# Kernel optimization log

Measured on AMD Instinct MI355X. Metric: run time of the kernel, lower is better.

The kernel has to match this reference:

```python
import jax, jax.numpy as jnp
import numpy as np

N = 100000  # number of nodes
E = 1600000  # number of edges (before self-loops)
D_IN, D_HID, D_OUT = 128, 128, 64


def gcn_conv(x, src, dst, W, b):
    """One PyG-style GCNConv: x' = D^{-1/2} A_hat D^{-1/2} (x W) + b, with self-loops in src/dst."""
    h = x @ W  # [N, D_out]
    deg = jax.ops.segment_sum(jnp.ones(src.shape[0], dtype=h.dtype), dst, num_segments=N)
    dinv = jnp.where(deg > 0, jax.lax.rsqrt(deg), 0.0)
    norm = dinv[src] * dinv[dst]  # [E+N]
    msgs = h[src] * norm[:, None]  # gather + scale
    out = jax.ops.segment_sum(msgs, dst, num_segments=N)  # scatter-add
    return out + b


def setup_inputs() -> dict:
    key = jax.random.key(0)
    k1, k2, k3, k4 = jax.random.split(key, 4)
    x = jax.random.normal(k1, (N, D_IN), dtype=jnp.float32)
    edge_index = jax.random.randint(k2, (2, E), 0, N, dtype=jnp.int64)
    W1 = jax.random.normal(k3, (D_IN, D_HID), dtype=jnp.float32) * (1.0 / np.sqrt(D_IN))
    b1 = jnp.zeros((D_HID,), dtype=jnp.float32)
    W2 = jax.random.normal(k4, (D_HID, D_OUT), dtype=jnp.float32) * (1.0 / np.sqrt(D_HID))
    b2 = jnp.zeros((D_OUT,), dtype=jnp.float32)
    return {"x": x, "edge_index": edge_index, "W1": W1, "b1": b1, "W2": W2, "b2": b2}


def reference(x, edge_index, W1, b1, W2, b2):
    # add self-loops once (GCNConv default add_self_loops=True)
    loops = jnp.arange(N, dtype=edge_index.dtype)
    src = jnp.concatenate([edge_index[0], loops])
    dst = jnp.concatenate([edge_index[1], loops])
    h = jax.nn.relu(gcn_conv(x, src, dst, W1, b1))
    out = gcn_conv(h, src, dst, W2, b2)
    return out
```

## Files before the change

kernel.cpp:

```cpp
#include <hip/hip_runtime.h>


#define NN 100000
#define EE 1600000
#define NB 391
#define BCAP 4608
#define PCAP 6656
#define EPB 8192
#define PBLK ((EE + EPB - 1) / EPB)

typedef _Float16 f16;
typedef _Float16 f16x8 __attribute__((ext_vector_type(8)));
typedef _Float16 f16x4 __attribute__((ext_vector_type(4)));
typedef float f32x4 __attribute__((ext_vector_type(4)));

__device__ __forceinline__ int load_idx(const void* p, long long i, int is64) {
    if (is64) return (int)((const long long*)p)[i];
    return ((const int*)p)[i];
}

__global__ void init_buckets(int* cursor) {
    int i = blockIdx.x * 256 + threadIdx.x;
    if (i < NB) cursor[i] = i * BCAP;
}

__global__ __launch_bounds__(256) void partition_kernel(const void* ei,
                                                        int* __restrict__ cursor,
                                                        unsigned* __restrict__ col32) {
    __shared__ int lh[NB], lbase[NB], lfill[NB];
    __shared__ int s_is64;
    for (int i = threadIdx.x; i < NB; i += 256) { lh[i] = 0; lfill[i] = 0; }
    if (threadIdx.x == 0) {
        const unsigned* w = (const unsigned*)ei;
        unsigned acc = 0;
        #pragma unroll
        for (int k = 0; k < 8; k++) acc |= w[2 * (k * 997 + 1) + 1];
        s_is64 = (acc == 0);
    }
    __syncthreads();
    int is64 = s_is64;
    long long base = (long long)blockIdx.x * EPB;
    #pragma unroll 4
    for (int k = 0; k < EPB / 256; k++) {
        long long i = base + k * 256 + threadIdx.x;
        if (i < EE) {
            int d = load_idx(ei, (long long)EE + i, is64);
            atomicAdd(&lh[d >> 8], 1);
        }
    }
    __syncthreads();
    for (int i = threadIdx.x; i < NB; i += 256)
        lbase[i] = lh[i] ? atomicAdd(&cursor[i], lh[i]) : 0;
    __syncthreads();
    #pragma unroll 4
    for (int k = 0; k < EPB / 256; k++) {
        long long i = base + k * 256 + threadIdx.x;
        if (i < EE) {
            int s = load_idx(ei, i, is64);
            int d = load_idx(ei, (long long)EE + i, is64);
            int b = d >> 8;
            int r = atomicAdd(&lfill[b], 1);
            col32[lbase[b] + r] = ((unsigned)s << 8) | (unsigned)(d & 255);
        }
    }
}

__global__ __launch_bounds__(256) void bucket_fill_kernel(const unsigned* __restrict__ col32,
                                                          const int* __restrict__ cursor,
                                                          int2* __restrict__ rsp,
                                                          float* __restrict__ dinv,
                                                          int* __restrict__ col) {
    __shared__ int cnt[256], incl[256], lfill[256];
    int t = threadIdx.x, b = blockIdx.x;
    cnt[t] = 0; lfill[t] = 0;
    __syncthreads();
    int base = b * BCAP;
    int end = cursor[b];
    for (int i = base + t; i < end; i += 256)
        atomicAdd(&cnt[col32[i] & 255u], 1);
    __syncthreads();
    int pc = (cnt[t] + 7) & ~7;
    incl[t] = pc;
    __syncthreads();
    #pragma unroll
    for (int off = 1; off < 256; off <<= 1) {
        int v = (t >= off) ? incl[t - off] : 0;
        __syncthreads();
        if (t >= off) incl[t] += v;
        __syncthreads();
    }
    int node = b * 256 + t;
    int excl = (t == 0) ? 0 : incl[t - 1];
    int myrs = b * PCAP + excl;
    if (node < NN) {
        rsp[node] = make_int2(myrs, pc);
        dinv[node] = rsqrtf((float)(cnt[t] + 1));
    }
    __syncthreads();
    for (int i = base + t; i < end; i += 256) {
        unsigned p = col32[i];
        int d = p & 255u;
        int r = atomicAdd(&lfill[d], 1);
        int ex = (d == 0) ? 0 : incl[d - 1];
        col[b * PCAP + ex + r] = (int)(p >> 8);
    }
    __syncthreads();
    int cn = cnt[t];
    for (int k = cn; k < pc; k++) col[myrs + k] = NN;
    if (t == 255) {
        int tot = incl[255];
        for (int k = 0; k < 8; k++) col[b * PCAP + tot + k] = NN;
    }
}

__global__ void prep_split(const float* __restrict__ W1, const float* __restrict__ W2,
                           f16* __restrict__ W1h, f16* __restrict__ W1l,
                           f16* __restrict__ W2h, f16* __restrict__ W2l) {
    int t = blockIdx.x * 256 + threadIdx.x;
    if (t < 128 * 128) {
        int k = t >> 7, n = t & 127;
        float v = W1[t];
        f16 h = (f16)v;
        f16 l = (f16)(v - (float)h);
        int idx = n * 128 + (k ^ ((n & 7) << 3));
        W1h[idx] = h; W1l[idx] = l;
    } else if (t < 128 * 128 + 128 * 64) {
        int u = t - 128 * 128;
        int k = u >> 6, n = u & 63;
        float v = W2[u];
        f16 h = (f16)v;
        f16 l = (f16)(v - (float)h);
        int idx = n * 128 + (k ^ ((n & 7) << 3));
        W2h[idx] = h; W2l[idx] = l;
    }
}

template <int M, int SPLIT_A>
__global__ __launch_bounds__(256) void gemm_mfma(const void* __restrict__ Xv,
                                                 const f16* __restrict__ Wh,
                                                 const f16* __restrict__ Wl,
                                                 const float* __restrict__ dinv,
                                                 f16* __restrict__ H) {
    __shared__ f16 wsh[M * 128];
    __shared__ f16 wsl[M * 128];
    const int tid = threadIdx.x;
    for (int c = tid; c < M * 16; c += 256) {
        *(float4*)&wsh[c * 8] = ((const float4*)Wh)[c];
        *(float4*)&wsl[c * 8] = ((const float4*)Wl)[c];
    }
    __syncthreads();

    const int lane = tid & 63;
    const int wv = tid >> 6;
    const int m0 = lane & 15;
    const int kg = lane >> 4;
    int row = blockIdx.x * 64 + wv * 16 + m0;
    if (row >= NN) row = NN - 1;

    constexpr int NT = M / 16;
    f32x4 acc[NT];
    #pragma unroll
    for (int i = 0; i < NT; i++) acc[i] = (f32x4){0.f, 0.f, 0.f, 0.f};

    #pragma unroll
    for (int kt = 0; kt < 4; ++kt) {
        int k0 = kt * 32 + kg * 8;
        f16x8 ah, al;
        if (SPLIT_A) {
            const float* xr = (const float*)Xv + (size_t)row * 128 + k0;
            float xv[8];
            *(float4*)&xv[0] = *(const float4*)xr;
            *(float4*)&xv[4] = *(const float4*)(xr + 4);
            #pragma unroll
            for (int r = 0; r < 8; r++) {
                ah[r] = (f16)xv[r];
                al[r] = (f16)(xv[r] - (float)ah[r]);
            }
        } else {
            ah = *(const f16x8*)((const f16*)Xv + (size_t)row * 128 + k0);
        }
        #pragma unroll
        for (int nt = 0; nt < NT; ++nt) {
            int n = nt * 16 + m0;
            int sch = (kt * 4 + kg) ^ (n & 7);
            int off = n * 128 + sch * 8;
            f16x8 bh = *(const f16x8*)&wsh[off];
            f16x8 bl = *(const f16x8*)&wsl[off];
            acc[nt] = __builtin_amdgcn_mfma_f32_16x16x32_f16(ah, bh, acc[nt], 0, 0, 0);
            if (SPLIT_A)
                acc[nt] = __builtin_amdgcn_mfma_f32_16x16x32_f16(al, bh, acc[nt], 0, 0, 0);
            acc[nt] = __builtin_amdgcn_mfma_f32_16x16x32_f16(ah, bl, acc[nt], 0, 0, 0);
        }
    }

    int r0 = blockIdx.x * 64 + wv * 16 + kg * 4;
    float dv[4];
    #pragma unroll
    for (int i = 0; i < 4; i++) {
        int r = r0 + i;
        dv[i] = (r < NN) ? dinv[r] : 0.f;
    }
    #pragma unroll
    for (int nt = 0; nt < NT; ++nt) {
        int cidx = nt * 16 + m0;
        #pragma unroll
        for (int i = 0; i < 4; i++) {
            int r = r0 + i;
            if (r < NN) H[(size_t)r * M + cidx] = (f16)(acc[nt][i] * dv[i]);
        }
    }
}

__global__ __launch_bounds__(256) void agg128(const f16* __restrict__ h,
                                              const int2* __restrict__ rsp,
                                              const int* __restrict__ col,
                                              const float* __restrict__ dinv,
                                              const float* __restrict__ bias,
                                              f16* __restrict__ out) {
    int node = (blockIdx.x * 256 + threadIdx.x) >> 6;
    if (node >= NN) return;
    int lane = threadIdx.x & 63;
    int grp = lane >> 4, gl = lane & 15;
    int2 g = rsp[node];
    int s = g.x, e = g.x + g.y;
    const f16x8* hp = (const f16x8*)h;
    float acc[8];
    #pragma unroll
    for (int k = 0; k < 8; k++) acc[k] = 0.f;
    int c0 = col[s + grp], c1 = col[s + 4 + grp];
    for (int j = s; j < e; j += 8) {
        int n0 = col[j + 8 + grp];
        int n1 = col[j + 12 + grp];
        f16x8 v0 = hp[(unsigned)(c0 * 16 + gl)];
        f16x8 v1 = hp[(unsigned)(c1 * 16 + gl)];
        #pragma unroll
        for (int k = 0; k < 8; k++) acc[k] += (float)v0[k];
        #pragma unroll
        for (int k = 0; k < 8; k++) acc[k] += (float)v1[k];
        c0 = n0; c1 = n1;
    }
    #pragma unroll
    for (int k = 0; k < 8; k++) acc[k] += __shfl_xor(acc[k], 32);
    #pragma unroll
    for (int k = 0; k < 8; k++) acc[k] += __shfl_xor(acc[k], 16);
    if (grp == 0) {
        f16x8 sv = hp[(unsigned)(node * 16 + gl)];
        float di = dinv[node];
        float4 b0 = ((const float4*)bias)[gl * 2];
        float4 b1 = ((const float4*)bias)[gl * 2 + 1];
        float bb[8] = {b0.x, b0.y, b0.z, b0.w, b1.x, b1.y, b1.z, b1.w};
        f16x8 o;
        #pragma unroll
        for (int k = 0; k < 8; k++) {
            float v = fmaf(acc[k] + (float)sv[k], di, bb[k]);
            o[k] = (f16)fmaxf(v, 0.f);
        }
        ((f16x8*)out)[(unsigned)(node * 16 + gl)] = o;
    }
}

__global__ __launch_bounds__(256) void agg64(const f16* __restrict__ h,
                                             const int2* __restrict__ rsp,
                                             const int* __restrict__ col,
                                             const float* __restrict__ dinv,
                                             const float* __restrict__ bias,
                                             float* __restrict__ out) {
    int node = (blockIdx.x * 256 + threadIdx.x) >> 6;
    if (node >= NN) return;
    int lane = threadIdx.x & 63;
    int grp = lane >> 4, gl = lane & 15;
    int2 g = rsp[node];
    int s = g.x, e = g.x + g.y;
    const f16x4* hp = (const f16x4*)h;
    float acc[4];
    #pragma unroll
    for (int k = 0; k < 4; k++) acc[k] = 0.f;
    int c0 = col[s + grp], c1 = col[s + 4 + grp];
    for (int j = s; j < e; j += 8) {
        int n0 = col[j + 8 + grp];
        int n1 = col[j + 12 + grp];
        f16x4 v0 = hp[(unsigned)(c0 * 16 + gl)];
        f16x4 v1 = hp[(unsigned)(c1 * 16 + gl)];
        #pragma unroll
        for (int k = 0; k < 4; k++) acc[k] += (float)v0[k];
        #pragma unroll
        for (int k = 0; k < 4; k++) acc[k] += (float)v1[k];
        c0 = n0; c1 = n1;
    }
    #pragma unroll
    for (int k = 0; k < 4; k++) acc[k] += __shfl_xor(acc[k], 32);
    #pragma unroll
    for (int k = 0; k < 4; k++) acc[k] += __shfl_xor(acc[k], 16);
    if (grp == 0) {
        f16x4 sv = hp[(unsigned)(node * 16 + gl)];
        float di = dinv[node];
        float4 b = ((const float4*)bias)[gl];
        float4 o;
        o.x = fmaf(acc[0] + (float)sv[0], di, b.x);
        o.y = fmaf(acc[1] + (float)sv[1], di, b.y);
        o.z = fmaf(acc[2] + (float)sv[2], di, b.z);
        o.w = fmaf(acc[3] + (float)sv[3], di, b.w);
        ((float4*)out)[(unsigned)(node * 16 + gl)] = o;
    }
}

extern "C" void kernel_launch(void* const* d_in, const int* in_sizes, int n_in,
                              void* d_out, int out_size, void* d_ws, size_t ws_size,
                              hipStream_t stream) {
    const float* x  = (const float*)d_in[0];
    const void*  ei = d_in[1];
    const float* W1 = (const float*)d_in[2];
    const float* b1 = (const float*)d_in[3];
    const float* W2 = (const float*)d_in[4];
    const float* b2 = (const float*)d_in[5];
    float* out = (float*)d_out;

    char* wsp = (char*)d_ws;
    size_t off = 0;
    auto alloc = [&](size_t bytes) {
        void* p = wsp + off;
        off += (bytes + 255) & ~(size_t)255;
        return p;
    };
    f16*      h1     = (f16*)alloc((size_t)(NN + 1) * 128 * 2);
    f16*      a1     = (f16*)alloc((size_t)NN * 128 * 2);
    f16*      h2     = (f16*)alloc((size_t)(NN + 1) * 64 * 2);
    int*      col    = (int*)alloc((size_t)NB * PCAP * 4);
    int2*     rsp    = (int2*)alloc((size_t)NN * 8);
    float*    dinv   = (float*)alloc((size_t)NN * 4);
    int*      cursor = (int*)alloc((size_t)NB * 4);
    f16*      W1h    = (f16*)alloc(128 * 128 * 2);
    f16*      W1l    = (f16*)alloc(128 * 128 * 2);
    f16*      W2h    = (f16*)alloc(64 * 128 * 2);
    f16*      W2l    = (f16*)alloc(64 * 128 * 2);
    unsigned* col32  = (unsigned*)a1;
    (void)ws_size; (void)in_sizes; (void)n_in; (void)out_size;

    hipMemsetAsync(h1 + (size_t)NN * 128, 0, 256, stream);
    hipMemsetAsync(h2 + (size_t)NN * 64, 0, 128, stream);

    prep_split<<<96, 256, 0, stream>>>(W1, W2, W1h, W1l, W2h, W2l);
    init_buckets<<<2, 256, 0, stream>>>(cursor);
    partition_kernel<<<PBLK, 256, 0, stream>>>(ei, cursor, col32);
    bucket_fill_kernel<<<NB, 256, 0, stream>>>(col32, cursor, rsp, dinv, col);

    gemm_mfma<128, 1><<<(NN + 63) / 64, 256, 0, stream>>>(x, W1h, W1l, dinv, h1);
    agg128<<<(NN * 64) / 256, 256, 0, stream>>>(h1, rsp, col, dinv, b1, a1);
    gemm_mfma<64, 0><<<(NN + 63) / 64, 256, 0, stream>>>(a1, W2h, W2l, dinv, h2);
    agg64<<<(NN * 64) / 256, 256, 0, stream>>>(h2, rsp, col, dinv, b2, out);
}
```

Measured before the change: 216.5 us.

## Unroll agg128 gathers to 16 edges and remap agg64 to half-wave per node

agg128 now handles 16 neighbours per iteration with two accumulator sets, so more independent row gathers are in flight. agg64 is restructured so 32 lanes cover one node's 64 features as f16x2 pairs and walk 8 neighbours per iteration with no cross-lane reduction, launching half the threads. The bucket padding is widened to 16 sentinel entries and the col allocation is enlarged to cover the deeper prefetch. The aim is more memory-level parallelism and fewer shuffles, at the cost of extra registers and narrower 4-byte loads per lane in agg64.

```diff
diff --git a/kernel.cpp b/kernel.cpp
--- a/kernel.cpp
+++ b/kernel.cpp
@@ -11,7 +11,7 @@
 
 typedef _Float16 f16;
 typedef _Float16 f16x8 __attribute__((ext_vector_type(8)));
-typedef _Float16 f16x4 __attribute__((ext_vector_type(4)));
+typedef _Float16 f16x2 __attribute__((ext_vector_type(2)));
 typedef float f32x4 __attribute__((ext_vector_type(4)));
 
 __device__ __forceinline__ int load_idx(const void* p, long long i, int is64) {
@@ -109,7 +109,7 @@
     for (int k = cn; k < pc; k++) col[myrs + k] = NN;
     if (t == 255) {
         int tot = incl[255];
-        for (int k = 0; k < 8; k++) col[b * PCAP + tot + k] = NN;
+        for (int k = 0; k < 16; k++) col[b * PCAP + tot + k] = NN;
     }
 }
 
@@ -224,21 +224,34 @@
     int2 g = rsp[node];
     int s = g.x, e = g.x + g.y;
     const f16x8* hp = (const f16x8*)h;
+    float accA[8], accB[8];
+    #pragma unroll
+    for (int k = 0; k < 8; k++) { accA[k] = 0.f; accB[k] = 0.f; }
+    int c0a = col[s + grp], c1a = col[s + 4 + grp];
+    int c0b = col[s + 8 + grp], c1b = col[s + 12 + grp];
+    int j = s;
+    for (; j + 16 <= e; j += 16) {
+        f16x8 v0 = hp[(unsigned)(c0a * 16 + gl)];
+        f16x8 v1 = hp[(unsigned)(c1a * 16 + gl)];
+        f16x8 v2 = hp[(unsigned)(c0b * 16 + gl)];
+        f16x8 v3 = hp[(unsigned)(c1b * 16 + gl)];
+        c0a = col[j + 16 + grp]; c1a = col[j + 20 + grp];
+        c0b = col[j + 24 + grp]; c1b = col[j + 28 + grp];
+        #pragma unroll
+        for (int k = 0; k < 8; k++) {
+            accA[k] += (float)v0[k] + (float)v1[k];
+            accB[k] += (float)v2[k] + (float)v3[k];
+        }
+    }
+    if (j < e) {
+        f16x8 v0 = hp[(unsigned)(c0a * 16 + gl)];
+        f16x8 v1 = hp[(unsigned)(c1a * 16 + gl)];
+        #pragma unroll
+        for (int k = 0; k < 8; k++) accA[k] += (float)v0[k] + (float)v1[k];
+    }
     float acc[8];
     #pragma unroll
-    for (int k = 0; k < 8; k++) acc[k] = 0.f;
-    int c0 = col[s + grp], c1 = col[s + 4 + grp];
-    for (int j = s; j < e; j += 8) {
-        int n0 = col[j + 8 + grp];
-        int n1 = col[j + 12 + grp];
-        f16x8 v0 = hp[(unsigned)(c0 * 16 + gl)];
-        f16x8 v1 = hp[(unsigned)(c1 * 16 + gl)];
-        #pragma unroll
-        for (int k = 0; k < 8; k++) acc[k] += (float)v0[k];
-        #pragma unroll
-        for (int k = 0; k < 8; k++) acc[k] += (float)v1[k];
-        c0 = n0; c1 = n1;
-    }
+    for (int k = 0; k < 8; k++) acc[k] = accA[k] + accB[k];
     #pragma unroll
     for (int k = 0; k < 8; k++) acc[k] += __shfl_xor(acc[k], 32);
     #pragma unroll
@@ -265,43 +278,44 @@
                                              const float* __restrict__ dinv,
                                              const float* __restrict__ bias,
                                              float* __restrict__ out) {
-    int node = (blockIdx.x * 256 + threadIdx.x) >> 6;
+    int node = (blockIdx.x * 256 + threadIdx.x) >> 5;
+    int lane = threadIdx.x & 31;
     if (node >= NN) return;
-    int lane = threadIdx.x & 63;
-    int grp = lane >> 4, gl = lane & 15;
+    float di = dinv[node];
+    const f16x2* hp = (const f16x2*)h;
+    f16x2 sv = hp[(unsigned)(node * 32 + lane)];
     int2 g = rsp[node];
     int s = g.x, e = g.x + g.y;
-    const f16x4* hp = (const f16x4*)h;
-    float acc[4];
-    #pragma unroll
-    for (int k = 0; k < 4; k++) acc[k] = 0.f;
-    int c0 = col[s + grp], c1 = col[s + 4 + grp];
+    float ax[8], ay[8];
+    #pragma unroll
+    for (int i = 0; i < 8; i++) { ax[i] = 0.f; ay[i] = 0.f; }
+    int c[8];
+    if (s < e) {
+        #pragma unroll
+        for (int i = 0; i < 8; i++) c[i] = col[s + i];
+    }
     for (int j = s; j < e; j += 8) {
-        int n0 = col[j + 8 + grp];
-        int n1 = col[j + 12 + grp];
-        f16x4 v0 = hp[(unsigned)(c0 * 16 + gl)];
-        f16x4 v1 = hp[(unsigned)(c1 * 16 + gl)];
-        #pragma unroll
-        for (int k = 0; k < 4; k++) acc[k] += (float)v0[k];
-        #pragma unroll
-        for (int k = 0; k < 4; k++) acc[k] += (float)v1[k];
-        c0 = n0; c1 = n1;
-    }
-    #pragma unroll
-    for (int k = 0; k < 4; k++) acc[k] += __shfl_xor(acc[k], 32);
-    #pragma unroll
-    for (int k = 0; k < 4; k++) acc[k] += __shfl_xor(acc[k], 16);
-    if (grp == 0) {
-        f16x4 sv = hp[(unsigned)(node * 16 + gl)];
-        float di = dinv[node];
-        float4 b = ((const float4*)bias)[gl];
-        float4 o;
-        o.x = fmaf(acc[0] + (float)sv[0], di, b.x);
-        o.y = fmaf(acc[1] + (float)sv[1], di, b.y);
-        o.z = fmaf(acc[2] + (float)sv[2], di, b.z);
-        o.w = fmaf(acc[3] + (float)sv[3], di, b.w);
-        ((float4*)out)[(unsigned)(node * 16 + gl)] = o;
-    }
+        int cn[8];
+        #pragma unroll
+        for (int i = 0; i < 8; i++) cn[i] = col[j + 8 + i];
+        f16x2 v[8];
+        #pragma unroll
+        for (int i = 0; i < 8; i++) v[i] = hp[(unsigned)(c[i] * 32 + lane)];
+        #pragma unroll
+        for (int i = 0; i < 8; i++) {
+            ax[i] += (float)v[i][0];
+            ay[i] += (float)v[i][1];
+        }
+        #pragma unroll
+        for (int i = 0; i < 8; i++) c[i] = cn[i];
+    }
+    float sx = ((ax[0] + ax[1]) + (ax[2] + ax[3])) + ((ax[4] + ax[5]) + (ax[6] + ax[7]));
+    float sy = ((ay[0] + ay[1]) + (ay[2] + ay[3])) + ((ay[4] + ay[5]) + (ay[6] + ay[7]));
+    sx += (float)sv[0];
+    sy += (float)sv[1];
+    float2 bv = ((const float2*)bias)[lane];
+    float2 o = make_float2(fmaf(sx, di, bv.x), fmaf(sy, di, bv.y));
+    ((float2*)(out + (size_t)node * 64))[lane] = o;
 }
 
 extern "C" void kernel_launch(void* const* d_in, const int* in_sizes, int n_in,
@@ -325,7 +339,7 @@
     f16*      h1     = (f16*)alloc((size_t)(NN + 1) * 128 * 2);
     f16*      a1     = (f16*)alloc((size_t)NN * 128 * 2);
     f16*      h2     = (f16*)alloc((size_t)(NN + 1) * 64 * 2);
-    int*      col    = (int*)alloc((size_t)NB * PCAP * 4);
+    int*      col    = (int*)alloc((size_t)(NB * PCAP + 64) * 4);
     int2*     rsp    = (int2*)alloc((size_t)NN * 8);
     float*    dinv   = (float*)alloc((size_t)NN * 4);
     int*      cursor = (int*)alloc((size_t)NB * 4);
@@ -347,5 +361,5 @@
     gemm_mfma<128, 1><<<(NN + 63) / 64, 256, 0, stream>>>(x, W1h, W1l, dinv, h1);
     agg128<<<(NN * 64) / 256, 256, 0, stream>>>(h1, rsp, col, dinv, b1, a1);
     gemm_mfma<64, 0><<<(NN + 63) / 64, 256, 0, stream>>>(a1, W2h, W2l, dinv, h2);
-    agg64<<<(NN * 64) / 256, 256, 0, stream>>>(h2, rsp, col, dinv, b2, out);
-}
+    agg64<<<(NN * 32 + 255) / 256, 256, 0, stream>>>(h2, rsp, col, dinv, b2, out);
+}
```

Measured after the change: 199.5 us. -7.9%, faster.
